# Kernel tuning notes

Measured on AMD Instinct MI355X. Metric: run time of the kernel, lower is better.

## Reference

```python
import jax, jax.numpy as jnp
from jax import lax
import numpy as np

ALPHA = 0.1  # topological regularization weight
INF = jnp.float32(1e30)


def _delay_embed(x):
    # Takens time-delay embedding, dimension 3, delay 1: [L] -> [L-2, 3]
    return jnp.stack([x[:-2], x[1:-1], x[2:]], axis=-1)


def _pdist(p):
    # Euclidean pairwise distances: [n,3] -> [n,n]
    sq = jnp.sum(p * p, axis=-1)
    d2 = sq[:, None] + sq[None, :] - 2.0 * (p @ p.T)
    return jnp.sqrt(jnp.maximum(d2, 0.0))


def _mst_deaths(D):
    # 0-dimensional Vietoris-Rips persistence death times = single-linkage
    # merge heights = MST edge weights. Dense Prim, O(n^2), sequential pairing
    # phase mirrors the per-sample CPU persistent-homology loop of the original.
    n = D.shape[0]
    visited = jnp.zeros((n,), dtype=bool).at[0].set(True)
    mind = D[0].at[0].set(INF)  # min distance from tree to each vertex
    deaths = jnp.zeros((n - 1,), dtype=D.dtype)

    def body(i, carry):
        mind, visited, deaths = carry
        cand = jnp.where(visited, INF, mind)
        j = jnp.argmin(cand)
        deaths = deaths.at[i].set(cand[j])
        visited = visited.at[j].set(True)
        mind = jnp.minimum(mind, D[j])
        return (mind, visited, deaths)

    _, _, deaths = lax.fori_loop(0, n - 1, body, (mind, visited, deaths))
    return deaths


def _topo_features(x):
    # x: [B, L] -> sorted (descending) persistence values per sample: [B, L-3]
    def one(series):
        D = _pdist(_delay_embed(series))
        return jnp.sort(_mst_deaths(D))[::-1]
    return jax.vmap(one)(x)


def setup_inputs() -> dict:
    key = jax.random.key(0)
    k1, k2 = jax.random.split(key)
    B, L = 32, 2048
    pred = jax.random.normal(k1, (B, L), dtype=jnp.float32)
    target = jax.random.normal(k2, (B, L), dtype=jnp.float32)
    return {"pred": pred, "target": target}


def reference(pred, target):
    mse_loss = jnp.mean((pred - target) ** 2)
    # topological features are computed on detached data in the original
    pred_topo = lax.stop_gradient(_topo_features(pred))
    target_topo = lax.stop_gradient(_topo_features(target))
    topo_loss = jnp.mean((pred_topo - target_topo) ** 2)
    return mse_loss + ALPHA * topo_loss
```

## Files before the change

kernel.cpp:

```cpp
#include <hip/hip_runtime.h>
#include <math.h>

#define LLEN 2048
#define BATCH 32
#define N_PTS (LLEN - 2)
#define N_DEATH (LLEN - 3)
#define SORT_N 2048
#define TPB 256
#define NW 4
#define BIG 1e30f
#define TOPO_BYTES ((size_t)64 * N_DEATH * 4)

typedef float v2f __attribute__((ext_vector_type(2)));

__device__ __forceinline__ unsigned dpp_umin6(unsigned v) {
    unsigned t;
    t = (unsigned)__builtin_amdgcn_update_dpp(-1, (int)v, 0x111, 0xF, 0xF, false);
    v = t < v ? t : v;
    t = (unsigned)__builtin_amdgcn_update_dpp(-1, (int)v, 0x112, 0xF, 0xF, false);
    v = t < v ? t : v;
    t = (unsigned)__builtin_amdgcn_update_dpp(-1, (int)v, 0x114, 0xF, 0xF, false);
    v = t < v ? t : v;
    t = (unsigned)__builtin_amdgcn_update_dpp(-1, (int)v, 0x118, 0xF, 0xF, false);
    v = t < v ? t : v;
    t = (unsigned)__builtin_amdgcn_update_dpp(-1, (int)v, 0x142, 0xF, 0xF, false);
    v = t < v ? t : v;
    t = (unsigned)__builtin_amdgcn_update_dpp(-1, (int)v, 0x143, 0xF, 0xF, false);
    v = t < v ? t : v;
    return v;
}

template<int PT, bool FIRST, bool COMPACT>
__device__ __forceinline__ void prim_phase(
    const int t, const int lane, const int wid,
    const int i0, const int i1, const unsigned rem_in,
    float4* __restrict__ pp, float* __restrict__ deaths,
    unsigned* __restrict__ xslot, unsigned* __restrict__ wtot,
    float& pjx, float& pjy, float& pjz)
{
    v2f px2[PT / 2], py2[PT / 2], pz2[PT / 2];
    unsigned m[PT];
    unsigned vis = 0u;
#pragma unroll
    for (int s = 0; s < PT; ++s) {
        const int idx = s * 256 + t;
        float4 p = pp[idx];
        if (s & 1) { px2[s >> 1].y = p.x; py2[s >> 1].y = p.y; pz2[s >> 1].y = p.z; }
        else       { px2[s >> 1].x = p.x; py2[s >> 1].x = p.y; pz2[s >> 1].x = p.z; }
        if (FIRST) {
            m[s] = 0x7F800000u | (unsigned)idx;
            if (idx >= (int)rem_in || idx == 0) vis |= 1u << s;
        } else {
            m[s] = __float_as_uint(p.w);
            if (idx >= (int)rem_in) vis |= 1u << s;
        }
    }

#pragma unroll 1
    for (int i = i0; i < i1; ++i) {
        v2f jx = {pjx, pjx}, jy = {pjy, pjy}, jz = {pjz, pjz};
        unsigned lv0 = 0xFFFFFFFFu, lv1 = 0xFFFFFFFFu;
#pragma unroll
        for (int k = 0; k < PT / 2; ++k) {
            v2f dx = px2[k] - jx, dy = py2[k] - jy, dz = pz2[k] - jz;
            v2f d2 = dx * dx + dy * dy + dz * dz;
            unsigned pk0 = (__float_as_uint(d2.x) & 0xFFFFF000u) | (unsigned)((2 * k) * 256 + t);
            unsigned pk1 = (__float_as_uint(d2.y) & 0xFFFFF000u) | (unsigned)((2 * k + 1) * 256 + t);
            unsigned nm0 = m[2 * k] < pk0 ? m[2 * k] : pk0;
            unsigned nm1 = m[2 * k + 1] < pk1 ? m[2 * k + 1] : pk1;
            m[2 * k] = nm0;
            m[2 * k + 1] = nm1;
            unsigned e0 = (unsigned)__builtin_amdgcn_sbfe((int)vis, 2 * k, 1);
            unsigned e1 = (unsigned)__builtin_amdgcn_sbfe((int)vis, 2 * k + 1, 1);
            unsigned c0 = nm0 | e0, c1 = nm1 | e1;
            lv0 = lv0 < c0 ? lv0 : c0;
            lv1 = lv1 < c1 ? lv1 : c1;
        }
        unsigned lv = lv0 < lv1 ? lv0 : lv1;
        unsigned wmin = dpp_umin6(lv);
        const int base = (i & 1) * NW;
        if (lane == 63) xslot[base + wid] = wmin;
        asm volatile("s_barrier" ::: "memory");
        const uint4 q = *(const uint4*)&xslot[base];
        unsigned w01 = q.x < q.y ? q.x : q.y;
        unsigned w23 = q.z < q.w ? q.z : q.w;
        unsigned win = w01 < w23 ? w01 : w23;
        int j = (int)(win & 0x7FFu);
        vis |= (t == (j & 255)) ? (1u << (j >> 8)) : 0u;
        float4 pj = pp[j];
        pjx = pj.x; pjy = pj.y; pjz = pj.z;
        if (t == 0) deaths[i] = __uint_as_float(win & 0xFFFFF000u);
    }

    if (COMPACT) {
        const unsigned livemask = ~vis & ((1u << PT) - 1u);
        const unsigned cnt = (unsigned)__popc(livemask);
        unsigned inc = cnt;
#pragma unroll
        for (int d = 1; d < 64; d <<= 1) {
            unsigned tt = (unsigned)__shfl_up((int)inc, d, 64);
            if (lane >= d) inc += tt;
        }
        if (lane == 63) wtot[wid] = inc;
        asm volatile("s_barrier" ::: "memory");
        unsigned wbase = 0;
#pragma unroll
        for (int w = 0; w < NW; ++w) wbase += (w < wid) ? wtot[w] : 0u;
        unsigned dst = wbase + inc - cnt;
#pragma unroll
        for (int s = 0; s < PT; ++s) {
            if ((livemask >> s) & 1u) {
                float xx = (s & 1) ? px2[s >> 1].y : px2[s >> 1].x;
                float yy = (s & 1) ? py2[s >> 1].y : py2[s >> 1].x;
                float zz = (s & 1) ? pz2[s >> 1].y : pz2[s >> 1].x;
                pp[dst] = make_float4(xx, yy, zz,
                                      __uint_as_float((m[s] & 0xFFFFF000u) | dst));
                ++dst;
            }
        }
        asm volatile("s_barrier" ::: "memory");
    }
}

__global__ __launch_bounds__(TPB)
void topo_kernel(const float* __restrict__ pred,
                 const float* __restrict__ tgt,
                 float* __restrict__ topo ,
                 unsigned* __restrict__ ctr,
                 int fuse,
                 float* __restrict__ out) {
    __shared__ float4 pp[SORT_N];
    __shared__ float deaths[SORT_N];
    __shared__ __align__(16) unsigned xslot[2 * NW];
    __shared__ unsigned wtot[NW];
    __shared__ unsigned lastflag;

    const int b = blockIdx.x;
    const float* x = (b < BATCH) ? (pred + b * LLEN) : (tgt + (b - BATCH) * LLEN);
    const int t = threadIdx.x;
    const int lane = t & 63;
    const int wid = t >> 6;

#pragma unroll
    for (int s = 0; s < 8; ++s) {
        int idx = s * 256 + t;
        bool valid = idx < N_PTS;
        float vx = valid ? x[idx]     : 0.f;
        float vy = valid ? x[idx + 1] : 0.f;
        float vz = valid ? x[idx + 2] : 0.f;
        pp[idx] = make_float4(vx, vy, vz, 0.f);
    }
    __syncthreads();

    float pjx = x[0], pjy = x[1], pjz = x[2];

    prim_phase<8, true,  true >(t, lane, wid, 0,    509,  N_PTS, pp, deaths, xslot, wtot, pjx, pjy, pjz);
    prim_phase<6, false, true >(t, lane, wid, 509,  1021, 1536,  pp, deaths, xslot, wtot, pjx, pjy, pjz);
    prim_phase<4, false, true >(t, lane, wid, 1021, 1533, 1024,  pp, deaths, xslot, wtot, pjx, pjy, pjz);
    prim_phase<2, false, false>(t, lane, wid, 1533, 2045, 512,   pp, deaths, xslot, wtot, pjx, pjy, pjz);

    if (t < SORT_N - N_DEATH) deaths[N_DEATH + t] = -BIG;
    __syncthreads();

    for (int k = 2; k <= SORT_N; k <<= 1) {
        for (int jj = k >> 1; jj > 0; jj >>= 1) {
#pragma unroll
            for (int s = 0; s < SORT_N / TPB; ++s) {
                int ii = t + s * TPB;
                int ixj = ii ^ jj;
                if (ixj > ii) {
                    float a = deaths[ii], c = deaths[ixj];
                    bool descBlock = ((ii & k) == 0);
                    bool doSwap = descBlock ? (a < c) : (a > c);
                    if (doSwap) { deaths[ii] = c; deaths[ixj] = a; }
                }
            }
            __syncthreads();
        }
    }

    for (int e = t; e < N_DEATH; e += TPB)
        topo[b * N_DEATH + e] = sqrtf(deaths[e]);

    if (!fuse) return;

    __syncthreads();
    if (t == 0) {
        __threadfence();
        unsigned prev = __hip_atomic_fetch_add(ctr, 1u, __ATOMIC_ACQ_REL,
                                               __HIP_MEMORY_SCOPE_AGENT);
        lastflag = (prev == 63u) ? 1u : 0u;
        __threadfence();
    }
    __syncthreads();
    if (lastflag == 0u) return;

    float msum = 0.f;
    const float4* p4 = (const float4*)pred;
    const float4* t4 = (const float4*)tgt;
    for (int e = t; e < (BATCH * LLEN) / 4; e += TPB) {
        float4 a = p4[e], c = t4[e];
        float dx = a.x - c.x, dy = a.y - c.y, dz = a.z - c.z, dw = a.w - c.w;
        msum += dx * dx + dy * dy + dz * dz + dw * dw;
    }
    float tsum = 0.f;
    const float4* q4 = (const float4*)topo;
    const int nt4 = (BATCH * N_DEATH) / 4;
    for (int e = t; e < nt4; e += TPB) {
        float4 a = q4[e], c = q4[e + nt4];
        float dx = a.x - c.x, dy = a.y - c.y, dz = a.z - c.z, dw = a.w - c.w;
        tsum += dx * dx + dy * dy + dz * dz + dw * dw;
    }
    __shared__ float sm[2][NW];
#pragma unroll
    for (int off = 32; off >= 1; off >>= 1) {
        msum += __shfl_xor(msum, off);
        tsum += __shfl_xor(tsum, off);
    }
    if (lane == 0) { sm[0][wid] = msum; sm[1][wid] = tsum; }
    __syncthreads();
    if (t == 0) {
        float M = 0.f, T = 0.f;
#pragma unroll
        for (int w = 0; w < NW; ++w) { M += sm[0][w]; T += sm[1][w]; }
        out[0] = M / (float)(BATCH * LLEN) + 0.1f * (T / (float)(BATCH * N_DEATH));
    }
}

#define RTPB 1024
__global__ __launch_bounds__(RTPB)
void loss_kernel(const float* __restrict__ pred,
                 const float* __restrict__ tgt,
                 const float* __restrict__ topo,
                 float* __restrict__ out) {
    const int t = threadIdx.x;
    float msum = 0.f;
    const float4* p4 = (const float4*)pred;
    const float4* t4 = (const float4*)tgt;
    const int n4 = (BATCH * LLEN) / 4;
    for (int e = t; e < n4; e += RTPB) {
        float4 a = p4[e], c = t4[e];
        float dx = a.x - c.x, dy = a.y - c.y, dz = a.z - c.z, dw = a.w - c.w;
        msum += dx * dx + dy * dy + dz * dz + dw * dw;
    }
    float tsum = 0.f;
    const int nt = BATCH * N_DEATH;
    for (int e = t; e < nt; e += RTPB) {
        float d = topo[e] - topo[e + nt];
        tsum += d * d;
    }
    __shared__ float sm[2][RTPB / 64];
#pragma unroll
    for (int off = 32; off >= 1; off >>= 1) {
        msum += __shfl_xor(msum, off);
        tsum += __shfl_xor(tsum, off);
    }
    int lane = t & 63, wid = t >> 6;
    if (lane == 0) { sm[0][wid] = msum; sm[1][wid] = tsum; }
    __syncthreads();
    if (t == 0) {
        float M = 0.f, T = 0.f;
#pragma unroll
        for (int w = 0; w < RTPB / 64; ++w) { M += sm[0][w]; T += sm[1][w]; }
        out[0] = M / (float)(BATCH * LLEN) + 0.1f * (T / (float)nt);
    }
}

extern "C" void kernel_launch(void* const* d_in, const int* in_sizes, int n_in,
                              void* d_out, int out_size, void* d_ws, size_t ws_size,
                              hipStream_t stream) {
    const float* pred = (const float*)d_in[0];
    const float* tgt  = (const float*)d_in[1];
    float* topo = (float*)d_ws;
    unsigned* ctr = (unsigned*)((char*)d_ws + TOPO_BYTES);
    const int fuse = (ws_size >= TOPO_BYTES + sizeof(unsigned)) ? 1 : 0;

    if (fuse) hipMemsetAsync(ctr, 0, sizeof(unsigned), stream);

    topo_kernel<<<2 * BATCH, TPB, 0, stream>>>(pred, tgt, topo,
                                               fuse ? ctr : nullptr, fuse,
                                               (float*)d_out);
    if (!fuse)
        loss_kernel<<<1, RTPB, 0, stream>>>(pred, tgt, topo, (float*)d_out);
}
```

Baseline: 631.3 us.

## Double block size to 512 threads and halve per-thread points in Prim loop

Raises threads per block from 256 to 512 (8 wavefronts), so each thread holds half as many points in registers during the sequential Prim iterations. The packed v2f arithmetic is replaced by scalar floats, and the cross-wave reduction now reads 8 slots instead of 4. The aim is a shorter per-iteration critical path in the 2045-step sequential loop. In exchange, each block barrier now synchronises more waves, the reduction is slightly longer, and packed-math throughput is lost.

```diff
diff --git a/kernel.cpp b/kernel.cpp
--- a/kernel.cpp
+++ b/kernel.cpp
@@ -6,12 +6,10 @@
 #define N_PTS (LLEN - 2)
 #define N_DEATH (LLEN - 3)
 #define SORT_N 2048
-#define TPB 256
-#define NW 4
+#define TPB 512
+#define NW 8
 #define BIG 1e30f
 #define TOPO_BYTES ((size_t)64 * N_DEATH * 4)
-
-typedef float v2f __attribute__((ext_vector_type(2)));
 
 __device__ __forceinline__ unsigned dpp_umin6(unsigned v) {
     unsigned t;
@@ -38,15 +36,14 @@
     unsigned* __restrict__ xslot, unsigned* __restrict__ wtot,
     float& pjx, float& pjy, float& pjz)
 {
-    v2f px2[PT / 2], py2[PT / 2], pz2[PT / 2];
+    float px[PT], py[PT], pz[PT];
     unsigned m[PT];
     unsigned vis = 0u;
 #pragma unroll
     for (int s = 0; s < PT; ++s) {
-        const int idx = s * 256 + t;
+        const int idx = s * TPB + t;
         float4 p = pp[idx];
-        if (s & 1) { px2[s >> 1].y = p.x; py2[s >> 1].y = p.y; pz2[s >> 1].y = p.z; }
-        else       { px2[s >> 1].x = p.x; py2[s >> 1].x = p.y; pz2[s >> 1].x = p.z; }
+        px[s] = p.x; py[s] = p.y; pz[s] = p.z;
         if (FIRST) {
             m[s] = 0x7F800000u | (unsigned)idx;
             if (idx >= (int)rem_in || idx == 0) vis |= 1u << s;
@@ -58,35 +55,35 @@
 
 #pragma unroll 1
     for (int i = i0; i < i1; ++i) {
-        v2f jx = {pjx, pjx}, jy = {pjy, pjy}, jz = {pjz, pjz};
         unsigned lv0 = 0xFFFFFFFFu, lv1 = 0xFFFFFFFFu;
 #pragma unroll
-        for (int k = 0; k < PT / 2; ++k) {
-            v2f dx = px2[k] - jx, dy = py2[k] - jy, dz = pz2[k] - jz;
-            v2f d2 = dx * dx + dy * dy + dz * dz;
-            unsigned pk0 = (__float_as_uint(d2.x) & 0xFFFFF000u) | (unsigned)((2 * k) * 256 + t);
-            unsigned pk1 = (__float_as_uint(d2.y) & 0xFFFFF000u) | (unsigned)((2 * k + 1) * 256 + t);
-            unsigned nm0 = m[2 * k] < pk0 ? m[2 * k] : pk0;
-            unsigned nm1 = m[2 * k + 1] < pk1 ? m[2 * k + 1] : pk1;
-            m[2 * k] = nm0;
-            m[2 * k + 1] = nm1;
-            unsigned e0 = (unsigned)__builtin_amdgcn_sbfe((int)vis, 2 * k, 1);
-            unsigned e1 = (unsigned)__builtin_amdgcn_sbfe((int)vis, 2 * k + 1, 1);
-            unsigned c0 = nm0 | e0, c1 = nm1 | e1;
-            lv0 = lv0 < c0 ? lv0 : c0;
-            lv1 = lv1 < c1 ? lv1 : c1;
+        for (int s = 0; s < PT; ++s) {
+            float dx = px[s] - pjx, dy = py[s] - pjy, dz = pz[s] - pjz;
+            float d2 = dx * dx + dy * dy + dz * dz;
+            unsigned pk = (__float_as_uint(d2) & 0xFFFFF000u) | (unsigned)(s * TPB + t);
+            unsigned nm = m[s] < pk ? m[s] : pk;
+            m[s] = nm;
+            unsigned ext = (unsigned)__builtin_amdgcn_sbfe((int)vis, s, 1);
+            unsigned cand = nm | ext;
+            if (s & 1) lv1 = lv1 < cand ? lv1 : cand;
+            else       lv0 = lv0 < cand ? lv0 : cand;
         }
         unsigned lv = lv0 < lv1 ? lv0 : lv1;
         unsigned wmin = dpp_umin6(lv);
         const int base = (i & 1) * NW;
         if (lane == 63) xslot[base + wid] = wmin;
         asm volatile("s_barrier" ::: "memory");
-        const uint4 q = *(const uint4*)&xslot[base];
-        unsigned w01 = q.x < q.y ? q.x : q.y;
-        unsigned w23 = q.z < q.w ? q.z : q.w;
-        unsigned win = w01 < w23 ? w01 : w23;
+        const uint4 qa = *(const uint4*)&xslot[base];
+        const uint4 qb = *(const uint4*)&xslot[base + 4];
+        unsigned w01 = qa.x < qa.y ? qa.x : qa.y;
+        unsigned w23 = qa.z < qa.w ? qa.z : qa.w;
+        unsigned w45 = qb.x < qb.y ? qb.x : qb.y;
+        unsigned w67 = qb.z < qb.w ? qb.z : qb.w;
+        unsigned wA = w01 < w23 ? w01 : w23;
+        unsigned wB = w45 < w67 ? w45 : w67;
+        unsigned win = wA < wB ? wA : wB;
         int j = (int)(win & 0x7FFu);
-        vis |= (t == (j & 255)) ? (1u << (j >> 8)) : 0u;
+        vis |= (t == (j & (TPB - 1))) ? (1u << (j >> 9)) : 0u;
         float4 pj = pp[j];
         pjx = pj.x; pjy = pj.y; pjz = pj.z;
         if (t == 0) deaths[i] = __uint_as_float(win & 0xFFFFF000u);
@@ -110,10 +107,7 @@
 #pragma unroll
         for (int s = 0; s < PT; ++s) {
             if ((livemask >> s) & 1u) {
-                float xx = (s & 1) ? px2[s >> 1].y : px2[s >> 1].x;
-                float yy = (s & 1) ? py2[s >> 1].y : py2[s >> 1].x;
-                float zz = (s & 1) ? pz2[s >> 1].y : pz2[s >> 1].x;
-                pp[dst] = make_float4(xx, yy, zz,
+                pp[dst] = make_float4(px[s], py[s], pz[s],
                                       __uint_as_float((m[s] & 0xFFFFF000u) | dst));
                 ++dst;
             }
@@ -142,8 +136,8 @@
     const int wid = t >> 6;
 
 #pragma unroll
-    for (int s = 0; s < 8; ++s) {
-        int idx = s * 256 + t;
+    for (int s = 0; s < 4; ++s) {
+        int idx = s * TPB + t;
         bool valid = idx < N_PTS;
         float vx = valid ? x[idx]     : 0.f;
         float vy = valid ? x[idx + 1] : 0.f;
@@ -154,10 +148,10 @@
 
     float pjx = x[0], pjy = x[1], pjz = x[2];
 
-    prim_phase<8, true,  true >(t, lane, wid, 0,    509,  N_PTS, pp, deaths, xslot, wtot, pjx, pjy, pjz);
-    prim_phase<6, false, true >(t, lane, wid, 509,  1021, 1536,  pp, deaths, xslot, wtot, pjx, pjy, pjz);
-    prim_phase<4, false, true >(t, lane, wid, 1021, 1533, 1024,  pp, deaths, xslot, wtot, pjx, pjy, pjz);
-    prim_phase<2, false, false>(t, lane, wid, 1533, 2045, 512,   pp, deaths, xslot, wtot, pjx, pjy, pjz);
+    prim_phase<4, true,  true >(t, lane, wid, 0,    509,  N_PTS, pp, deaths, xslot, wtot, pjx, pjy, pjz);
+    prim_phase<3, false, true >(t, lane, wid, 509,  1021, 1536,  pp, deaths, xslot, wtot, pjx, pjy, pjz);
+    prim_phase<2, false, true >(t, lane, wid, 1021, 1533, 1024,  pp, deaths, xslot, wtot, pjx, pjy, pjz);
+    prim_phase<1, false, false>(t, lane, wid, 1533, 2045, 512,   pp, deaths, xslot, wtot, pjx, pjy, pjz);
 
     if (t < SORT_N - N_DEATH) deaths[N_DEATH + t] = -BIG;
     __syncthreads();
```

Measured after the change: 698.4 us. 1.11x slower.
